# Kernel tuning notes

Hardware: AMD Instinct MI355X
Metric: run time of the kernel (lower is better)

The kernel has to match this reference:

```python
import jax, jax.numpy as jnp
import numpy as np

# Dimensions (decode path: seq_len == 1)
NS, SL = 32, 1            # num_seqs, query seq_len
NH, KVH, HS = 32, 8, 128  # query heads, kv heads, head size
QPK = NH // KVH           # queries per kv head (GQA)
X = 8                     # vLLM key-cache vectorization factor
NB, BS = 4096, 16         # num cache blocks, block_size
MB = 128                  # max blocks per sequence -> max_context_len = MB*BS = 2048
SCALE = 1.0 / float(np.sqrt(HS))


def setup_inputs() -> dict:
    key = jax.random.key(0)
    ks = jax.random.split(key, 6)
    query = jax.random.normal(ks[0], (NS, SL, NH * HS), jnp.float32)
    k_new = jax.random.normal(ks[1], (NS, SL, KVH * HS), jnp.float32)
    v_new = jax.random.normal(ks[2], (NS, SL, KVH * HS), jnp.float32)
    key_cache = jax.random.normal(ks[3], (NB, KVH, HS // X, BS, X), jnp.float32)
    value_cache = jax.random.normal(ks[4], (NB, KVH, HS, BS), jnp.float32)
    # disjoint block assignment: seq n owns blocks [n*MB, (n+1)*MB)
    block_tables = jnp.arange(NS * MB, dtype=jnp.int32).reshape(NS, MB)
    context_lens = jax.random.randint(ks[5], (NS,), 1, MB * BS + 1, jnp.int32)
    last = context_lens - 1  # position of the token being written this step
    slot_mapping = (block_tables[jnp.arange(NS), last // BS] * BS + last % BS)
    slot_mapping = slot_mapping.reshape(NS, SL).astype(jnp.int32)
    return dict(query=query, key=k_new, value=v_new, key_cache=key_cache,
                value_cache=value_cache, block_tables=block_tables,
                context_lens=context_lens, slot_mapping=slot_mapping)


def reference(query, key, value, key_cache, value_cache, block_tables,
              context_lens, slot_mapping):
    ns, sl, _ = query.shape
    q = query.reshape(ns * sl, NH, HS)
    k_new = key.reshape(ns * sl, KVH, HS)
    v_new = value.reshape(ns * sl, KVH, HS)
    slots = slot_mapping.reshape(-1)
    blk, off = slots // BS, slots % BS
    # reshape_and_cache: scatter new K/V into paged caches
    # key_cache[b, h, d, s, x] stores head-dim index d*X + x
    kc = key_cache.at[blk, :, :, off, :].set(k_new.reshape(-1, KVH, HS // X, X))
    vc = value_cache.at[blk, :, :, off].set(v_new)
    # reconstruct contiguous layout [NB, BS, KVH, HS]
    K = jnp.transpose(kc, (0, 3, 1, 2, 4)).reshape(NB, BS, KVH, HS)
    V = jnp.transpose(vc, (0, 3, 1, 2))
    # paged gather via block tables -> per-seq KV [ns, MB*BS, KVH, HS]
    Kg = K[block_tables].reshape(ns, MB * BS, KVH, HS)
    Vg = V[block_tables].reshape(ns, MB * BS, KVH, HS)
    # GQA attention: group query heads by kv head
    qr = q.reshape(ns, KVH, QPK, HS)
    scores = jnp.einsum('nkqd,nlkd->nkql', qr, Kg) * SCALE
    mask = jnp.arange(MB * BS)[None, :] < context_lens[:, None]  # [ns, L]
    scores = jnp.where(mask[:, None, None, :], scores, -jnp.inf)
    p = jax.nn.softmax(scores, axis=-1)
    out = jnp.einsum('nkql,nlkd->nkqd', p, Vg)
    return out.reshape(ns, sl, NH * HS)
```

## Files before the change

kernel.cpp:

```cpp
#include <hip/hip_runtime.h>
#include <math.h>

#define NSQ   32
#define NHQ   32
#define KVHN  8
#define HSZ   128
#define QPK   4
#define BSZ   16
#define MBL   128
#define LMAX  2048
#define SPLIT 128
#define NSPLIT (LMAX / SPLIT)
#define KSCALE 0.08838834764831843f

#define OPART_FLOATS (NSQ * KVHN * NSPLIT * QPK * HSZ)

typedef float f4 __attribute__((ext_vector_type(4)));

__device__ __forceinline__ f4 ntl4(const float* p) {
    return __builtin_nontemporal_load((const f4*)p);
}

__device__ __forceinline__ void vload16(const float* vp, f4& r0, f4& r1, f4& r2, f4& r3) {
    r0 = ntl4(vp); r1 = ntl4(vp + 4); r2 = ntl4(vp + 8); r3 = ntl4(vp + 12);
}

__device__ __forceinline__ void vfma16(const f4* scb, f4 r0, f4 r1, f4 r2, f4 r3,
                                       float& o0, float& o1, float& o2, float& o3) {
    #pragma unroll
    for (int s = 0; s < 4; ++s) { f4 p = scb[s];
        o0 += p[0]*r0[s]; o1 += p[1]*r0[s]; o2 += p[2]*r0[s]; o3 += p[3]*r0[s]; }
    #pragma unroll
    for (int s = 0; s < 4; ++s) { f4 p = scb[4+s];
        o0 += p[0]*r1[s]; o1 += p[1]*r1[s]; o2 += p[2]*r1[s]; o3 += p[3]*r1[s]; }
    #pragma unroll
    for (int s = 0; s < 4; ++s) { f4 p = scb[8+s];
        o0 += p[0]*r2[s]; o1 += p[1]*r2[s]; o2 += p[2]*r2[s]; o3 += p[3]*r2[s]; }
    #pragma unroll
    for (int s = 0; s < 4; ++s) { f4 p = scb[12+s];
        o0 += p[0]*r3[s]; o1 += p[1]*r3[s]; o2 += p[2]*r3[s]; o3 += p[3]*r3[s]; }
}

__global__ __launch_bounds__(128) void pa_attn_split(
    const float* __restrict__ query,
    const float* __restrict__ key,
    const float* __restrict__ value,
    const float* __restrict__ kc,
    const float* __restrict__ vc,
    const int* __restrict__ block_tables,
    const int* __restrict__ context_lens,
    float* __restrict__ opart,
    float* __restrict__ ml)
{
    const int wg    = blockIdx.x;
    const int split = wg >> 8;
    const int sk    = wg & 255;
    const int seq   = sk >> 3;
    const int kvh   = sk & 7;
    const int ctx   = context_lens[seq];
    const int start = split * SPLIT;
    if (start >= ctx) return;
    const int nvalid = min(SPLIT, ctx - start);

    __shared__ f4    sc4[SPLIT];
    __shared__ float redmax[2][QPK];
    __shared__ float redsum[2][QPK];

    const int t = threadIdx.x;
    const int g = start + t;

    const int* btrow = block_tables + seq * MBL + (start >> 4);
    const int bt0 = btrow[0], bt1 = btrow[1], bt2 = btrow[2], bt3 = btrow[3],
              bt4 = btrow[4], bt5 = btrow[5], bt6 = btrow[6], bt7 = btrow[7];

    const int nblk = (nvalid + 15) >> 4;
    const int d = t;
    const float* vbase = vc + (size_t)kvh * 2048 + (size_t)d * 16;

    f4 A0, A1, A2, A3, B0, B1, B2, B3;
    vload16(vbase + (size_t)bt0 * 16384, A0, A1, A2, A3);
    if (nblk > 1) vload16(vbase + (size_t)bt1 * 16384, B0, B1, B2, B3);

    const int qkblk = btrow[t >> 4];
    const float* kp;
    int kstr;
    if (g == ctx - 1) {
        kp   = key + seq * (KVHN*HSZ) + kvh * HSZ;
        kstr = 8;
    } else {
        kp   = kc + (size_t)qkblk * 16384 + kvh * 2048 + (t & 15) * 8;
        kstr = 128;
    }
    const f4* qb = (const f4*)(query + seq * (NHQ*HSZ) + (kvh * QPK) * HSZ);

    float acc[QPK] = {0.f, 0.f, 0.f, 0.f};
    #pragma unroll
    for (int d2 = 0; d2 < 16; ++d2) {
        f4 k0 = ntl4(kp);
        f4 k1 = ntl4(kp + 4);
        kp += kstr;
        #pragma unroll
        for (int h = 0; h < QPK; ++h) {
            f4 q0 = qb[h * 32 + d2 * 2];
            f4 q1 = qb[h * 32 + d2 * 2 + 1];
            acc[h] += k0[0]*q0[0] + k0[1]*q0[1] + k0[2]*q0[2] + k0[3]*q0[3]
                    + k1[0]*q1[0] + k1[1]*q1[1] + k1[2]*q1[2] + k1[3]*q1[3];
        }
    }
    const bool valid = (t < nvalid);
    float score[QPK];
    #pragma unroll
    for (int h = 0; h < QPK; ++h)
        score[h] = valid ? acc[h] * KSCALE : -INFINITY;

    float vmax[QPK];
    #pragma unroll
    for (int h = 0; h < QPK; ++h) {
        vmax[h] = score[h];
        #pragma unroll
        for (int off = 32; off > 0; off >>= 1)
            vmax[h] = fmaxf(vmax[h], __shfl_down(vmax[h], off));
    }
    const int wave = t >> 6, lane = t & 63;
    if (lane == 0) {
        #pragma unroll
        for (int h = 0; h < QPK; ++h) redmax[wave][h] = vmax[h];
    }
    __syncthreads();
    float mx[QPK];
    #pragma unroll
    for (int h = 0; h < QPK; ++h)
        mx[h] = fmaxf(redmax[0][h], redmax[1][h]);

    float e[QPK];
    #pragma unroll
    for (int h = 0; h < QPK; ++h)
        e[h] = valid ? __expf(score[h] - mx[h]) : 0.0f;
    { f4 ev = {e[0], e[1], e[2], e[3]}; sc4[t] = ev; }
    float lsum[QPK];
    #pragma unroll
    for (int h = 0; h < QPK; ++h) {
        lsum[h] = e[h];
        #pragma unroll
        for (int off = 32; off > 0; off >>= 1)
            lsum[h] += __shfl_down(lsum[h], off);
    }
    if (lane == 0) {
        #pragma unroll
        for (int h = 0; h < QPK; ++h) redsum[wave][h] = lsum[h];
    }
    __syncthreads();

    const int part_idx = (seq * KVHN + kvh) * NSPLIT + split;
    if (t < QPK) {
        ml[part_idx * QPK * 2 + t * 2 + 0] = mx[t];
        ml[part_idx * QPK * 2 + t * 2 + 1] = redsum[0][t] + redsum[1][t];
    }

    float o0 = 0.f, o1 = 0.f, o2 = 0.f, o3 = 0.f;

    if (nblk > 2) { f4 t0,t1,t2,t3; vload16(vbase + (size_t)bt2 * 16384, t0,t1,t2,t3);
                    vfma16(&sc4[0],  A0, A1, A2, A3, o0, o1, o2, o3); A0=t0;A1=t1;A2=t2;A3=t3; }
    else            vfma16(&sc4[0],  A0, A1, A2, A3, o0, o1, o2, o3);
    if (nblk > 3) { f4 t0,t1,t2,t3; vload16(vbase + (size_t)bt3 * 16384, t0,t1,t2,t3);
                    vfma16(&sc4[16], B0, B1, B2, B3, o0, o1, o2, o3); B0=t0;B1=t1;B2=t2;B3=t3; }
    else if (nblk > 1) vfma16(&sc4[16], B0, B1, B2, B3, o0, o1, o2, o3);
    if (nblk > 4) { f4 t0,t1,t2,t3; vload16(vbase + (size_t)bt4 * 16384, t0,t1,t2,t3);
                    vfma16(&sc4[32], A0, A1, A2, A3, o0, o1, o2, o3); A0=t0;A1=t1;A2=t2;A3=t3; }
    else if (nblk > 2) vfma16(&sc4[32], A0, A1, A2, A3, o0, o1, o2, o3);
    if (nblk > 5) { f4 t0,t1,t2,t3; vload16(vbase + (size_t)bt5 * 16384, t0,t1,t2,t3);
                    vfma16(&sc4[48], B0, B1, B2, B3, o0, o1, o2, o3); B0=t0;B1=t1;B2=t2;B3=t3; }
    else if (nblk > 3) vfma16(&sc4[48], B0, B1, B2, B3, o0, o1, o2, o3);
    if (nblk > 6) { f4 t0,t1,t2,t3; vload16(vbase + (size_t)bt6 * 16384, t0,t1,t2,t3);
                    vfma16(&sc4[64], A0, A1, A2, A3, o0, o1, o2, o3); A0=t0;A1=t1;A2=t2;A3=t3; }
    else if (nblk > 4) vfma16(&sc4[64], A0, A1, A2, A3, o0, o1, o2, o3);
    if (nblk > 7) { f4 t0,t1,t2,t3; vload16(vbase + (size_t)bt7 * 16384, t0,t1,t2,t3);
                    vfma16(&sc4[80], B0, B1, B2, B3, o0, o1, o2, o3); B0=t0;B1=t1;B2=t2;B3=t3; }
    else if (nblk > 5) vfma16(&sc4[80], B0, B1, B2, B3, o0, o1, o2, o3);
    if (nblk > 6)      vfma16(&sc4[96],  A0, A1, A2, A3, o0, o1, o2, o3);
    if (nblk > 7)      vfma16(&sc4[112], B0, B1, B2, B3, o0, o1, o2, o3);

    const int gl = ctx - 1;
    if (gl >= start && gl < start + SPLIT) {
        const int lo = gl - start;
        const int lb = lo >> 4, ls = lo & 15;
        const int vb = btrow[lb];
        const float vold = vc[(size_t)vb * 16384 + (size_t)kvh * 2048 + (size_t)d * 16 + ls];
        const float vnew = value[seq * (KVHN*HSZ) + kvh * HSZ + d];
        const f4 p = sc4[lo];
        const float dv = vnew - vold;
        o0 += p[0]*dv; o1 += p[1]*dv; o2 += p[2]*dv; o3 += p[3]*dv;
    }

    float* op = opart + (size_t)part_idx * (QPK * HSZ);
    op[0*HSZ + d] = o0; op[1*HSZ + d] = o1; op[2*HSZ + d] = o2; op[3*HSZ + d] = o3;
}

__global__ __launch_bounds__(128) void pa_combine(
    const float* __restrict__ opart,
    const float* __restrict__ ml,
    const int* __restrict__ context_lens,
    float* __restrict__ out)
{
    const int seq = blockIdx.x >> 3;
    const int kvh = blockIdx.x & 7;
    const int t   = threadIdx.x;
    const int ctx = context_lens[seq];
    const int nact = (ctx + SPLIT - 1) / SPLIT;
    const int part0 = (seq * KVHN + kvh) * NSPLIT;

    __shared__ float s_scale[NSPLIT][QPK];
    __shared__ float s_inv[QPK];

    if (t < 64) {
        const int h = t >> 4, s = t & 15;
        float m = -INFINITY, l = 0.0f;
        if (s < nact) {
            const float* mlp = ml + (size_t)(part0 + s) * (QPK*2) + h * 2;
            m = mlp[0]; l = mlp[1];
        }
        float M = m;
        #pragma unroll
        for (int off = 8; off > 0; off >>= 1)
            M = fmaxf(M, __shfl_xor(M, off));
        const float sc = (s < nact) ? __expf(m - M) : 0.0f;
        float dp = sc * l;
        #pragma unroll
        for (int off = 8; off > 0; off >>= 1)
            dp += __shfl_xor(dp, off);
        s_scale[s][h] = sc;
        if (s == 0) s_inv[h] = 1.0f / dp;
    }
    __syncthreads();

    float n0 = 0.f, n1 = 0.f, n2 = 0.f, n3 = 0.f;
    const float* opb = opart + (size_t)part0 * (QPK * HSZ) + t;
    for (int s = 0; s < nact; ++s) {
        const float* op = opb + (size_t)s * (QPK * HSZ);
        n0 += s_scale[s][0] * op[0*HSZ];
        n1 += s_scale[s][1] * op[1*HSZ];
        n2 += s_scale[s][2] * op[2*HSZ];
        n3 += s_scale[s][3] * op[3*HSZ];
    }
    float* ob = out + seq * (NHQ*HSZ) + (kvh * QPK) * HSZ + t;
    ob[0*HSZ] = n0 * s_inv[0];
    ob[1*HSZ] = n1 * s_inv[1];
    ob[2*HSZ] = n2 * s_inv[2];
    ob[3*HSZ] = n3 * s_inv[3];
}

extern "C" void kernel_launch(void* const* d_in, const int* in_sizes, int n_in,
                              void* d_out, int out_size, void* d_ws, size_t ws_size,
                              hipStream_t stream) {
    (void)in_sizes; (void)n_in; (void)ws_size; (void)out_size;
    const float* query        = (const float*)d_in[0];
    const float* key          = (const float*)d_in[1];
    const float* value        = (const float*)d_in[2];
    const float* key_cache    = (const float*)d_in[3];
    const float* value_cache  = (const float*)d_in[4];
    const int*   block_tables = (const int*)d_in[5];
    const int*   context_lens = (const int*)d_in[6];
    const int*   slot_mapping = (const int*)d_in[7];
    float*       out          = (float*)d_out;
    (void)slot_mapping;

    float* opart = (float*)d_ws;
    float* ml    = opart + OPART_FLOATS;

    hipLaunchKernelGGL(pa_attn_split, dim3(NSPLIT * NSQ * KVHN), dim3(SPLIT), 0, stream,
                       query, key, value, key_cache, value_cache, block_tables,
                       context_lens, opart, ml);
    hipLaunchKernelGGL(pa_combine, dim3(NSQ * KVHN), dim3(128), 0, stream,
                       opart, ml, context_lens, out);
}
```

Baseline: 479.3 us.

## Fuse split-KV attention and combine into single online-softmax kernel

Replaces the split-KV attention kernel and separate combine kernel with one kernel per (sequence, kv-head) that loops over 512-token tiles using an online softmax rescale. Each 512-thread workgroup splits the value accumulation across four thread quarters and sums them in shared memory at the end. This removes the second launch and the partial-output workspace round trip, at the cost of far fewer workgroups, serial tile iteration and load imbalance across variable context lengths.

```diff
diff --git a/kernel.cpp b/kernel.cpp
--- a/kernel.cpp
+++ b/kernel.cpp
@@ -9,11 +9,10 @@
 #define BSZ   16
 #define MBL   128
 #define LMAX  2048
-#define SPLIT 128
-#define NSPLIT (LMAX / SPLIT)
+#define TILE  512
+#define TBLK  (TILE/BSZ)
 #define KSCALE 0.08838834764831843f
 
-#define OPART_FLOATS (NSQ * KVHN * NSPLIT * QPK * HSZ)
 
 typedef float f4 __attribute__((ext_vector_type(4)));
 
@@ -41,7 +40,7 @@
         o0 += p[0]*r3[s]; o1 += p[1]*r3[s]; o2 += p[2]*r3[s]; o3 += p[3]*r3[s]; }
 }
 
-__global__ __launch_bounds__(128) void pa_attn_split(
+__global__ __launch_bounds__(512) void pa_fused(
     const float* __restrict__ query,
     const float* __restrict__ key,
     const float* __restrict__ value,
@@ -49,210 +48,181 @@
     const float* __restrict__ vc,
     const int* __restrict__ block_tables,
     const int* __restrict__ context_lens,
-    float* __restrict__ opart,
-    float* __restrict__ ml)
-{
-    const int wg    = blockIdx.x;
-    const int split = wg >> 8;
-    const int sk    = wg & 255;
-    const int seq   = sk >> 3;
-    const int kvh   = sk & 7;
-    const int ctx   = context_lens[seq];
-    const int start = split * SPLIT;
-    if (start >= ctx) return;
-    const int nvalid = min(SPLIT, ctx - start);
-
-    __shared__ f4    sc4[SPLIT];
-    __shared__ float redmax[2][QPK];
-    __shared__ float redsum[2][QPK];
-
-    const int t = threadIdx.x;
-    const int g = start + t;
-
-    const int* btrow = block_tables + seq * MBL + (start >> 4);
-    const int bt0 = btrow[0], bt1 = btrow[1], bt2 = btrow[2], bt3 = btrow[3],
-              bt4 = btrow[4], bt5 = btrow[5], bt6 = btrow[6], bt7 = btrow[7];
-
-    const int nblk = (nvalid + 15) >> 4;
-    const int d = t;
-    const float* vbase = vc + (size_t)kvh * 2048 + (size_t)d * 16;
-
-    f4 A0, A1, A2, A3, B0, B1, B2, B3;
-    vload16(vbase + (size_t)bt0 * 16384, A0, A1, A2, A3);
-    if (nblk > 1) vload16(vbase + (size_t)bt1 * 16384, B0, B1, B2, B3);
-
-    const int qkblk = btrow[t >> 4];
-    const float* kp;
-    int kstr;
-    if (g == ctx - 1) {
-        kp   = key + seq * (KVHN*HSZ) + kvh * HSZ;
-        kstr = 8;
-    } else {
-        kp   = kc + (size_t)qkblk * 16384 + kvh * 2048 + (t & 15) * 8;
-        kstr = 128;
-    }
-    const f4* qb = (const f4*)(query + seq * (NHQ*HSZ) + (kvh * QPK) * HSZ);
-
-    float acc[QPK] = {0.f, 0.f, 0.f, 0.f};
-    #pragma unroll
-    for (int d2 = 0; d2 < 16; ++d2) {
-        f4 k0 = ntl4(kp);
-        f4 k1 = ntl4(kp + 4);
-        kp += kstr;
-        #pragma unroll
-        for (int h = 0; h < QPK; ++h) {
-            f4 q0 = qb[h * 32 + d2 * 2];
-            f4 q1 = qb[h * 32 + d2 * 2 + 1];
-            acc[h] += k0[0]*q0[0] + k0[1]*q0[1] + k0[2]*q0[2] + k0[3]*q0[3]
-                    + k1[0]*q1[0] + k1[1]*q1[1] + k1[2]*q1[2] + k1[3]*q1[3];
-        }
-    }
-    const bool valid = (t < nvalid);
-    float score[QPK];
-    #pragma unroll
-    for (int h = 0; h < QPK; ++h)
-        score[h] = valid ? acc[h] * KSCALE : -INFINITY;
-
-    float vmax[QPK];
-    #pragma unroll
-    for (int h = 0; h < QPK; ++h) {
-        vmax[h] = score[h];
-        #pragma unroll
-        for (int off = 32; off > 0; off >>= 1)
-            vmax[h] = fmaxf(vmax[h], __shfl_down(vmax[h], off));
-    }
-    const int wave = t >> 6, lane = t & 63;
-    if (lane == 0) {
-        #pragma unroll
-        for (int h = 0; h < QPK; ++h) redmax[wave][h] = vmax[h];
-    }
-    __syncthreads();
-    float mx[QPK];
-    #pragma unroll
-    for (int h = 0; h < QPK; ++h)
-        mx[h] = fmaxf(redmax[0][h], redmax[1][h]);
-
-    float e[QPK];
-    #pragma unroll
-    for (int h = 0; h < QPK; ++h)
-        e[h] = valid ? __expf(score[h] - mx[h]) : 0.0f;
-    { f4 ev = {e[0], e[1], e[2], e[3]}; sc4[t] = ev; }
-    float lsum[QPK];
-    #pragma unroll
-    for (int h = 0; h < QPK; ++h) {
-        lsum[h] = e[h];
-        #pragma unroll
-        for (int off = 32; off > 0; off >>= 1)
-            lsum[h] += __shfl_down(lsum[h], off);
-    }
-    if (lane == 0) {
-        #pragma unroll
-        for (int h = 0; h < QPK; ++h) redsum[wave][h] = lsum[h];
-    }
-    __syncthreads();
-
-    const int part_idx = (seq * KVHN + kvh) * NSPLIT + split;
-    if (t < QPK) {
-        ml[part_idx * QPK * 2 + t * 2 + 0] = mx[t];
-        ml[part_idx * QPK * 2 + t * 2 + 1] = redsum[0][t] + redsum[1][t];
-    }
-
-    float o0 = 0.f, o1 = 0.f, o2 = 0.f, o3 = 0.f;
-
-    if (nblk > 2) { f4 t0,t1,t2,t3; vload16(vbase + (size_t)bt2 * 16384, t0,t1,t2,t3);
-                    vfma16(&sc4[0],  A0, A1, A2, A3, o0, o1, o2, o3); A0=t0;A1=t1;A2=t2;A3=t3; }
-    else            vfma16(&sc4[0],  A0, A1, A2, A3, o0, o1, o2, o3);
-    if (nblk > 3) { f4 t0,t1,t2,t3; vload16(vbase + (size_t)bt3 * 16384, t0,t1,t2,t3);
-                    vfma16(&sc4[16], B0, B1, B2, B3, o0, o1, o2, o3); B0=t0;B1=t1;B2=t2;B3=t3; }
-    else if (nblk > 1) vfma16(&sc4[16], B0, B1, B2, B3, o0, o1, o2, o3);
-    if (nblk > 4) { f4 t0,t1,t2,t3; vload16(vbase + (size_t)bt4 * 16384, t0,t1,t2,t3);
-                    vfma16(&sc4[32], A0, A1, A2, A3, o0, o1, o2, o3); A0=t0;A1=t1;A2=t2;A3=t3; }
-    else if (nblk > 2) vfma16(&sc4[32], A0, A1, A2, A3, o0, o1, o2, o3);
-    if (nblk > 5) { f4 t0,t1,t2,t3; vload16(vbase + (size_t)bt5 * 16384, t0,t1,t2,t3);
-                    vfma16(&sc4[48], B0, B1, B2, B3, o0, o1, o2, o3); B0=t0;B1=t1;B2=t2;B3=t3; }
-    else if (nblk > 3) vfma16(&sc4[48], B0, B1, B2, B3, o0, o1, o2, o3);
-    if (nblk > 6) { f4 t0,t1,t2,t3; vload16(vbase + (size_t)bt6 * 16384, t0,t1,t2,t3);
-                    vfma16(&sc4[64], A0, A1, A2, A3, o0, o1, o2, o3); A0=t0;A1=t1;A2=t2;A3=t3; }
-    else if (nblk > 4) vfma16(&sc4[64], A0, A1, A2, A3, o0, o1, o2, o3);
-    if (nblk > 7) { f4 t0,t1,t2,t3; vload16(vbase + (size_t)bt7 * 16384, t0,t1,t2,t3);
-                    vfma16(&sc4[80], B0, B1, B2, B3, o0, o1, o2, o3); B0=t0;B1=t1;B2=t2;B3=t3; }
-    else if (nblk > 5) vfma16(&sc4[80], B0, B1, B2, B3, o0, o1, o2, o3);
-    if (nblk > 6)      vfma16(&sc4[96],  A0, A1, A2, A3, o0, o1, o2, o3);
-    if (nblk > 7)      vfma16(&sc4[112], B0, B1, B2, B3, o0, o1, o2, o3);
-
-    const int gl = ctx - 1;
-    if (gl >= start && gl < start + SPLIT) {
-        const int lo = gl - start;
-        const int lb = lo >> 4, ls = lo & 15;
-        const int vb = btrow[lb];
-        const float vold = vc[(size_t)vb * 16384 + (size_t)kvh * 2048 + (size_t)d * 16 + ls];
-        const float vnew = value[seq * (KVHN*HSZ) + kvh * HSZ + d];
-        const f4 p = sc4[lo];
-        const float dv = vnew - vold;
-        o0 += p[0]*dv; o1 += p[1]*dv; o2 += p[2]*dv; o3 += p[3]*dv;
-    }
-
-    float* op = opart + (size_t)part_idx * (QPK * HSZ);
-    op[0*HSZ + d] = o0; op[1*HSZ + d] = o1; op[2*HSZ + d] = o2; op[3*HSZ + d] = o3;
-}
-
-__global__ __launch_bounds__(128) void pa_combine(
-    const float* __restrict__ opart,
-    const float* __restrict__ ml,
-    const int* __restrict__ context_lens,
     float* __restrict__ out)
 {
     const int seq = blockIdx.x >> 3;
     const int kvh = blockIdx.x & 7;
-    const int t   = threadIdx.x;
     const int ctx = context_lens[seq];
-    const int nact = (ctx + SPLIT - 1) / SPLIT;
-    const int part0 = (seq * KVHN + kvh) * NSPLIT;
-
-    __shared__ float s_scale[NSPLIT][QPK];
-    __shared__ float s_inv[QPK];
-
-    if (t < 64) {
-        const int h = t >> 4, s = t & 15;
-        float m = -INFINITY, l = 0.0f;
-        if (s < nact) {
-            const float* mlp = ml + (size_t)(part0 + s) * (QPK*2) + h * 2;
-            m = mlp[0]; l = mlp[1];
-        }
-        float M = m;
-        #pragma unroll
-        for (int off = 8; off > 0; off >>= 1)
-            M = fmaxf(M, __shfl_xor(M, off));
-        const float sc = (s < nact) ? __expf(m - M) : 0.0f;
-        float dp = sc * l;
-        #pragma unroll
-        for (int off = 8; off > 0; off >>= 1)
-            dp += __shfl_xor(dp, off);
-        s_scale[s][h] = sc;
-        if (s == 0) s_inv[h] = 1.0f / dp;
+    const int ntiles = (ctx + TILE - 1) / TILE;
+
+    __shared__ f4    sc4[TILE];
+    __shared__ float redmax[8][QPK];
+    __shared__ float redsum[8][QPK];
+    __shared__ float ocomb[4][QPK][HSZ];
+
+    const int t    = threadIdx.x;
+    const int wave = t >> 6, lane = t & 63;
+    const int d    = t & 127;
+    const int q4   = t >> 7;
+
+    const int* btrow = block_tables + seq * MBL;
+    const f4* qb = (const f4*)(query + seq * (NHQ*HSZ) + (kvh * QPK) * HSZ);
+    const float* vbase = vc + (size_t)kvh * 2048 + (size_t)d * 16;
+
+    float m[QPK], l[QPK];
+    float o0 = 0.f, o1 = 0.f, o2 = 0.f, o3 = 0.f;
+    #pragma unroll
+    for (int h = 0; h < QPK; ++h) { m[h] = -INFINITY; l[h] = 0.f; }
+
+    for (int ti = 0; ti < ntiles; ++ti) {
+        const int tb   = ti * TILE;
+        const int vtok = ctx - tb;
+        const int nvb  = min((vtok + 15) >> 4, TBLK);
+        const int nbq  = min(max(nvb - q4 * 8, 0), 8);
+        const int bq0  = ti * TBLK + q4 * 8;
+
+        f4 A0, A1, A2, A3, B0, B1, B2, B3;
+        if (nbq > 0) vload16(vbase + (size_t)btrow[bq0 + 0] * 16384, A0, A1, A2, A3);
+        if (nbq > 1) vload16(vbase + (size_t)btrow[bq0 + 1] * 16384, B0, B1, B2, B3);
+
+        const int g = tb + t;
+        const bool valid = (g < ctx);
+        float acc[QPK] = {0.f, 0.f, 0.f, 0.f};
+        if (valid) {
+            const float* kp; int kstr;
+            if (g == ctx - 1) {
+                kp   = key + seq * (KVHN*HSZ) + kvh * HSZ;
+                kstr = 8;
+            } else {
+                kp   = kc + (size_t)btrow[ti * TBLK + (t >> 4)] * 16384
+                          + kvh * 2048 + (t & 15) * 8;
+                kstr = 128;
+            }
+            #pragma unroll
+            for (int d2 = 0; d2 < 16; ++d2) {
+                f4 k0 = ntl4(kp);
+                f4 k1 = ntl4(kp + 4);
+                kp += kstr;
+                #pragma unroll
+                for (int h = 0; h < QPK; ++h) {
+                    f4 q0 = qb[h * 32 + d2 * 2];
+                    f4 q1 = qb[h * 32 + d2 * 2 + 1];
+                    acc[h] += k0[0]*q0[0] + k0[1]*q0[1] + k0[2]*q0[2] + k0[3]*q0[3]
+                            + k1[0]*q1[0] + k1[1]*q1[1] + k1[2]*q1[2] + k1[3]*q1[3];
+                }
+            }
+        }
+        float score[QPK];
+        #pragma unroll
+        for (int h = 0; h < QPK; ++h)
+            score[h] = valid ? acc[h] * KSCALE : -INFINITY;
+
+        float vmax[QPK];
+        #pragma unroll
+        for (int h = 0; h < QPK; ++h) {
+            vmax[h] = score[h];
+            #pragma unroll
+            for (int off = 32; off > 0; off >>= 1)
+                vmax[h] = fmaxf(vmax[h], __shfl_down(vmax[h], off));
+        }
+        if (lane == 0) {
+            #pragma unroll
+            for (int h = 0; h < QPK; ++h) redmax[wave][h] = vmax[h];
+        }
+        __syncthreads();
+        float mn[QPK], r[QPK];
+        #pragma unroll
+        for (int h = 0; h < QPK; ++h) {
+            float tm = redmax[0][h];
+            #pragma unroll
+            for (int w = 1; w < 8; ++w) tm = fmaxf(tm, redmax[w][h]);
+            mn[h] = fmaxf(m[h], tm);
+            r[h]  = __expf(m[h] - mn[h]);
+        }
+
+        float e[QPK];
+        #pragma unroll
+        for (int h = 0; h < QPK; ++h)
+            e[h] = valid ? __expf(score[h] - mn[h]) : 0.0f;
+        { f4 ev = {e[0], e[1], e[2], e[3]}; sc4[t] = ev; }
+        float lsum[QPK];
+        #pragma unroll
+        for (int h = 0; h < QPK; ++h) {
+            lsum[h] = e[h];
+            #pragma unroll
+            for (int off = 32; off > 0; off >>= 1)
+                lsum[h] += __shfl_down(lsum[h], off);
+        }
+        if (lane == 0) {
+            #pragma unroll
+            for (int h = 0; h < QPK; ++h) redsum[wave][h] = lsum[h];
+        }
+        __syncthreads();
+        #pragma unroll
+        for (int h = 0; h < QPK; ++h) {
+            float ts = redsum[0][h];
+            #pragma unroll
+            for (int w = 1; w < 8; ++w) ts += redsum[w][h];
+            l[h] = l[h] * r[h] + ts;
+            m[h] = mn[h];
+        }
+        o0 *= r[0]; o1 *= r[1]; o2 *= r[2]; o3 *= r[3];
+
+        const f4* scq = &sc4[q4 * 128];
+        if (nbq > 2) { f4 t0,t1,t2,t3; vload16(vbase + (size_t)btrow[bq0+2]*16384, t0,t1,t2,t3);
+                       vfma16(&scq[0],  A0,A1,A2,A3, o0,o1,o2,o3); A0=t0;A1=t1;A2=t2;A3=t3; }
+        else if (nbq > 0) vfma16(&scq[0],  A0,A1,A2,A3, o0,o1,o2,o3);
+        if (nbq > 3) { f4 t0,t1,t2,t3; vload16(vbase + (size_t)btrow[bq0+3]*16384, t0,t1,t2,t3);
+                       vfma16(&scq[16], B0,B1,B2,B3, o0,o1,o2,o3); B0=t0;B1=t1;B2=t2;B3=t3; }
+        else if (nbq > 1) vfma16(&scq[16], B0,B1,B2,B3, o0,o1,o2,o3);
+        if (nbq > 4) { f4 t0,t1,t2,t3; vload16(vbase + (size_t)btrow[bq0+4]*16384, t0,t1,t2,t3);
+                       vfma16(&scq[32], A0,A1,A2,A3, o0,o1,o2,o3); A0=t0;A1=t1;A2=t2;A3=t3; }
+        else if (nbq > 2) vfma16(&scq[32], A0,A1,A2,A3, o0,o1,o2,o3);
+        if (nbq > 5) { f4 t0,t1,t2,t3; vload16(vbase + (size_t)btrow[bq0+5]*16384, t0,t1,t2,t3);
+                       vfma16(&scq[48], B0,B1,B2,B3, o0,o1,o2,o3); B0=t0;B1=t1;B2=t2;B3=t3; }
+        else if (nbq > 3) vfma16(&scq[48], B0,B1,B2,B3, o0,o1,o2,o3);
+        if (nbq > 6) { f4 t0,t1,t2,t3; vload16(vbase + (size_t)btrow[bq0+6]*16384, t0,t1,t2,t3);
+                       vfma16(&scq[64], A0,A1,A2,A3, o0,o1,o2,o3); A0=t0;A1=t1;A2=t2;A3=t3; }
+        else if (nbq > 4) vfma16(&scq[64], A0,A1,A2,A3, o0,o1,o2,o3);
+        if (nbq > 7) { f4 t0,t1,t2,t3; vload16(vbase + (size_t)btrow[bq0+7]*16384, t0,t1,t2,t3);
+                       vfma16(&scq[80], B0,B1,B2,B3, o0,o1,o2,o3); B0=t0;B1=t1;B2=t2;B3=t3; }
+        else if (nbq > 5) vfma16(&scq[80], B0,B1,B2,B3, o0,o1,o2,o3);
+        if (nbq > 6)      vfma16(&scq[96],  A0,A1,A2,A3, o0,o1,o2,o3);
+        if (nbq > 7)      vfma16(&scq[112], B0,B1,B2,B3, o0,o1,o2,o3);
+
+        const int gl = ctx - 1;
+        if (gl >= tb && gl < tb + TILE) {
+            const int lo = gl - tb;
+            const int lb = lo >> 4;
+            if ((lb >> 3) == q4) {
+                const float vold = vc[(size_t)btrow[ti * TBLK + lb] * 16384
+                                      + (size_t)kvh * 2048 + (size_t)d * 16 + (lo & 15)];
+                const float vnew = value[seq * (KVHN*HSZ) + kvh * HSZ + d];
+                const f4 p = sc4[lo];
+                const float dv = vnew - vold;
+                o0 += p[0]*dv; o1 += p[1]*dv; o2 += p[2]*dv; o3 += p[3]*dv;
+            }
+        }
     }
+
+    ocomb[q4][0][d] = o0; ocomb[q4][1][d] = o1;
+    ocomb[q4][2][d] = o2; ocomb[q4][3][d] = o3;
     __syncthreads();
-
-    float n0 = 0.f, n1 = 0.f, n2 = 0.f, n3 = 0.f;
-    const float* opb = opart + (size_t)part0 * (QPK * HSZ) + t;
-    for (int s = 0; s < nact; ++s) {
-        const float* op = opb + (size_t)s * (QPK * HSZ);
-        n0 += s_scale[s][0] * op[0*HSZ];
-        n1 += s_scale[s][1] * op[1*HSZ];
-        n2 += s_scale[s][2] * op[2*HSZ];
-        n3 += s_scale[s][3] * op[3*HSZ];
+    if (q4 == 0) {
+        float* ob = out + seq * (NHQ*HSZ) + (kvh * QPK) * HSZ + d;
+        #pragma unroll
+        for (int h = 0; h < QPK; ++h) {
+            const float num = ocomb[0][h][d] + ocomb[1][h][d]
+                            + ocomb[2][h][d] + ocomb[3][h][d];
+            ob[h * HSZ] = num * (1.0f / l[h]);
+        }
     }
-    float* ob = out + seq * (NHQ*HSZ) + (kvh * QPK) * HSZ + t;
-    ob[0*HSZ] = n0 * s_inv[0];
-    ob[1*HSZ] = n1 * s_inv[1];
-    ob[2*HSZ] = n2 * s_inv[2];
-    ob[3*HSZ] = n3 * s_inv[3];
 }
 
 extern "C" void kernel_launch(void* const* d_in, const int* in_sizes, int n_in,
                               void* d_out, int out_size, void* d_ws, size_t ws_size,
                               hipStream_t stream) {
-    (void)in_sizes; (void)n_in; (void)ws_size; (void)out_size;
+    (void)in_sizes; (void)n_in; (void)ws_size; (void)out_size; (void)d_ws;
     const float* query        = (const float*)d_in[0];
     const float* key          = (const float*)d_in[1];
     const float* value        = (const float*)d_in[2];
@@ -264,12 +234,7 @@
     float*       out          = (float*)d_out;
     (void)slot_mapping;
 
-    float* opart = (float*)d_ws;
-    float* ml    = opart + OPART_FLOATS;
-
-    hipLaunchKernelGGL(pa_attn_split, dim3(NSPLIT * NSQ * KVHN), dim3(SPLIT), 0, stream,
-                       query, key, value, key_cache, value_cache, block_tables,
-                       context_lens, opart, ml);
-    hipLaunchKernelGGL(pa_combine, dim3(NSQ * KVHN), dim3(128), 0, stream,
-                       opart, ml, context_lens, out);
-}
+    hipLaunchKernelGGL(pa_fused, dim3(NSQ * KVHN), dim3(512), 0, stream,
+                       query, key, value, key_cache, value_cache,
+                       block_tables, context_lens, out);
+}
```

Result: slower. 519.2 us (+8.3%).
